# Performance work log

Measured on AMD Instinct MI355X. Metric: run time of the kernel, lower is better.

The kernel has to match this reference:

```python
import jax, jax.numpy as jnp
import numpy as np

N_NODES = 50000
N_EDGES = 800000
NUM_RELS = 16
IN_DIM, H_DIM, OUT_DIM = 128, 128, 64


def setup_inputs() -> dict:
    key = jax.random.key(0)
    ks = jax.random.split(key, 7)
    feat = jax.random.normal(ks[0], (N_NODES, IN_DIM), dtype=jnp.float32)
    norm = jax.random.uniform(ks[1], (N_EDGES, 1), dtype=jnp.float32)
    bound1 = 1.0 / np.sqrt(IN_DIM)
    bound2 = 1.0 / np.sqrt(H_DIM)
    W1 = jax.random.uniform(ks[2], (NUM_RELS, IN_DIM, H_DIM), dtype=jnp.float32, minval=-bound1, maxval=bound1)
    W2 = jax.random.uniform(ks[3], (NUM_RELS, H_DIM, OUT_DIM), dtype=jnp.float32, minval=-bound2, maxval=bound2)
    src = jax.random.randint(ks[4], (N_EDGES,), 0, N_NODES, dtype=jnp.int32)
    dst = jax.random.randint(ks[5], (N_EDGES,), 0, N_NODES, dtype=jnp.int32)
    etypes = jax.random.randint(ks[6], (N_EDGES,), 0, NUM_RELS, dtype=jnp.int32)
    return {"feat": feat, "norm": norm, "W1": W1, "W2": W2, "src": src, "dst": dst, "etypes": etypes}


def _rgcn_layer(h, W, src, dst, etypes, norm, num_nodes):
    # Transform every node by every relation weight (dense batched GEMM),
    # then gather the (src, etype) slice per edge: identical math to
    # gather_mm(h[src], W, idx_b=etypes) since matmul commutes with gather.
    t = jnp.einsum('ni,rio->nro', h, W)          # [N, R, O]
    msg = t[src, etypes] * norm                  # [E, O]
    return jax.ops.segment_sum(msg, dst, num_segments=num_nodes)  # sum-aggregate


def reference(feat, norm, W1, W2, src, dst, etypes):
    n = feat.shape[0]
    h = jax.nn.relu(_rgcn_layer(feat, W1, src, dst, etypes, norm, n))
    out = _rgcn_layer(h, W2, src, dst, etypes, norm, n)
    return out
```

## Files before the change

kernel.cpp:

```cpp
#include <hip/hip_runtime.h>


#define R_NUM 16

typedef __attribute__((ext_vector_type(8))) short bf16x8;
typedef __attribute__((ext_vector_type(4))) float f32x4;

__device__ __forceinline__ float bf2f(unsigned short u) {
    unsigned int x = ((unsigned int)u) << 16;
    return __builtin_bit_cast(float, x);
}
__device__ __forceinline__ unsigned short f2bf(float f) {
    unsigned int x = __builtin_bit_cast(unsigned int, f);
    x += 0x7FFFu + ((x >> 16) & 1u);
    return (unsigned short)(x >> 16);
}
__device__ __forceinline__ unsigned pack2(float a, float b) {
    return (unsigned)f2bf(a) | ((unsigned)f2bf(b) << 16);
}
__device__ __forceinline__ float lo16(unsigned v) { return bf2f((unsigned short)(v & 0xFFFF)); }
__device__ __forceinline__ float hi16(unsigned v) { return bf2f((unsigned short)(v >> 16)); }

__global__ void detect_dtype(const unsigned short* __restrict__ raw, int* flag) {
    __shared__ int tot;
    if (threadIdx.x == 0) tot = 0;
    __syncthreads();
    int c = 0;
    for (int i = threadIdx.x; i < 4096; i += 256) {
        unsigned short u = raw[2 * i];
        int e = (u >> 7) & 0xFF;
        if (e >= 113 && e <= 134) c++;
    }
    atomicAdd(&tot, c);
    __syncthreads();
    if (threadIdx.x == 0) *flag = (tot > 2048) ? 1 : 0;
}

__global__ void transpose_both(const void* __restrict__ W1, const void* __restrict__ W2,
                               unsigned short* __restrict__ w1t, unsigned short* __restrict__ w2t,
                               const int* __restrict__ flagp) {
    const int flag = *flagp;
    const int n1 = R_NUM * 128 * 128;
    const int n2 = R_NUM * 128 * 64;
    int idx = blockIdx.x * 256 + threadIdx.x;
    if (idx < n1) {
        int k = idx % 128, o = (idx / 128) % 128, r = idx / (128 * 128);
        int iin = (r * 128 + k) * 128 + o;
        float v = flag ? bf2f(((const unsigned short*)W1)[iin]) : ((const float*)W1)[iin];
        w1t[idx] = f2bf(v);
    } else if (idx < n1 + n2) {
        int j = idx - n1;
        int k = j % 128, o = (j / 128) % 64, r = j / (128 * 64);
        int iin = (r * 128 + k) * 64 + o;
        float v = flag ? bf2f(((const unsigned short*)W2)[iin]) : ((const float*)W2)[iin];
        w2t[j] = f2bf(v);
    }
}

template <int NOUT, int AMODE>
__global__ __launch_bounds__(256, 3) void gemm_all(const void* __restrict__ Asrc,
                                                   const unsigned short* __restrict__ Wt,
                                                   unsigned short* __restrict__ T, int nnodes,
                                                   const int* __restrict__ flagp) {
    constexpr int LDA = 136;
    constexpr int NTC = NOUT / 64;
    __shared__ unsigned short lA[64 * LDA];
    __shared__ unsigned short lB[NOUT * LDA];
    const int tid = threadIdx.x;
    const int node0 = blockIdx.x * 64;
    const int flag = (AMODE == 0) ? *flagp : 1;

    for (int i = tid; i < 64 * 16; i += 256) {
        int row = i >> 4, seg = i & 15;
        int node = node0 + row;
        uint4 v = make_uint4(0u, 0u, 0u, 0u);
        if (node < nnodes) {
            if (AMODE == 2 || flag) {
                v = *(const uint4*)((const unsigned short*)Asrc + (size_t)node * 128 + seg * 8);
            } else {
                const float* p = (const float*)Asrc + (size_t)node * 128 + seg * 8;
                float4 f0 = ((const float4*)p)[0];
                float4 f1 = ((const float4*)p)[1];
                v.x = pack2(f0.x, f0.y);
                v.y = pack2(f0.z, f0.w);
                v.z = pack2(f1.x, f1.y);
                v.w = pack2(f1.z, f1.w);
            }
        }
        *(uint4*)(lA + row * LDA + seg * 8) = v;
    }

    auto stageB = [&](int rel) {
        for (int i = tid; i < NOUT * 16; i += 256) {
            int o = i >> 4, seg = i & 15;
            *(uint4*)(lB + o * LDA + seg * 8) =
                *(const uint4*)(Wt + ((size_t)rel * NOUT + o) * 128 + seg * 8);
        }
    };
    stageB(0);
    __syncthreads();

    const int w = tid >> 6, lane = tid & 63;
    const int quad = lane >> 4, mr = lane & 15;

    bf16x8 afr[16];
#pragma unroll
    for (int mt = 0; mt < 4; mt++)
#pragma unroll
        for (int kk = 0; kk < 4; kk++)
            afr[mt * 4 + kk] = *(const bf16x8*)(lA + (mt * 16 + mr) * LDA + kk * 32 + quad * 8);

    constexpr int SEGS = NOUT / 8;
    constexpr int SPT = 64 * SEGS / 256;

    for (int rel = 0; rel < R_NUM; rel++) {
        f32x4 acc[4][NTC];
#pragma unroll
        for (int mt = 0; mt < 4; mt++)
#pragma unroll
            for (int c = 0; c < NTC; c++) acc[mt][c] = 0.f;

#pragma unroll
        for (int kk = 0; kk < 4; kk++) {
#pragma unroll
            for (int c = 0; c < NTC; c++) {
                bf16x8 b = *(const bf16x8*)(lB + (c * 64 + w * 16 + mr) * LDA + kk * 32 + quad * 8);
#pragma unroll
                for (int mt = 0; mt < 4; mt++)
                    acc[mt][c] = __builtin_amdgcn_mfma_f32_16x16x32_bf16(b, afr[mt * 4 + kk],
                                                                         acc[mt][c], 0, 0, 0);
            }
        }
        __syncthreads();

        if (rel + 1 < R_NUM) stageB(rel + 1);
#pragma unroll
        for (int mt = 0; mt < 4; mt++)
#pragma unroll
            for (int c = 0; c < NTC; c++) {
                uint2 pv;
                pv.x = pack2(acc[mt][c][0], acc[mt][c][1]);
                pv.y = pack2(acc[mt][c][2], acc[mt][c][3]);
                *(uint2*)(lA + (mt * 16 + mr) * LDA + c * 64 + w * 16 + quad * 4) = pv;
            }
        __syncthreads();

#pragma unroll
        for (int it = 0; it < SPT; it++) {
            int i = it * 256 + tid;
            int row = i / SEGS, seg = i % SEGS;
            int node = node0 + row;
            if (node < nnodes)
                *(uint4*)(T + ((size_t)rel * nnodes + node) * NOUT + seg * 8) =
                    *(const uint4*)(lA + row * LDA + seg * 8);
        }
    }
}

__global__ void hist_dst(const int* __restrict__ dst, int* __restrict__ counts, int nedges) {
    int e = blockIdx.x * 256 + threadIdx.x;
    if (e < nedges) atomicAdd(&counts[dst[e]], 1);
}

__global__ __launch_bounds__(256) void scan_phase1(const int* __restrict__ counts,
                                                   int* __restrict__ blocksums, int n) {
    __shared__ int red[256];
    int base = blockIdx.x * 1024 + threadIdx.x * 4;
    int s = 0;
#pragma unroll
    for (int j = 0; j < 4; j++) {
        int idx = base + j;
        if (idx < n) s += counts[idx];
    }
    red[threadIdx.x] = s;
    __syncthreads();
    for (int d = 128; d > 0; d >>= 1) {
        if (threadIdx.x < d) red[threadIdx.x] += red[threadIdx.x + d];
        __syncthreads();
    }
    if (threadIdx.x == 0) blocksums[blockIdx.x] = red[0];
}

__global__ __launch_bounds__(1024) void scan_phase2(const int* __restrict__ blocksums,
                                                    int* __restrict__ blockoff, int nb) {
    __shared__ int arr[1024];
    int t = threadIdx.x;
    arr[t] = (t < nb) ? blocksums[t] : 0;
    __syncthreads();
    for (int d = 1; d < 1024; d <<= 1) {
        int v = (t >= d) ? arr[t - d] : 0;
        __syncthreads();
        arr[t] += v;
        __syncthreads();
    }
    if (t < nb) blockoff[t] = (t == 0) ? 0 : arr[t - 1];
}

__global__ __launch_bounds__(256) void scan_phase3(const int* __restrict__ counts,
                                                   const int* __restrict__ blockoff,
                                                   int* __restrict__ offsets,
                                                   int* __restrict__ cursor, int n) {
    __shared__ int tsum[256];
    int base = blockIdx.x * 1024 + threadIdx.x * 4;
    int c[4];
    int s = 0;
#pragma unroll
    for (int j = 0; j < 4; j++) {
        int idx = base + j;
        c[j] = (idx < n) ? counts[idx] : 0;
        s += c[j];
    }
    tsum[threadIdx.x] = s;
    __syncthreads();
    for (int d = 1; d < 256; d <<= 1) {
        int v = (threadIdx.x >= d) ? tsum[threadIdx.x - d] : 0;
        __syncthreads();
        tsum[threadIdx.x] += v;
        __syncthreads();
    }
    int run = blockoff[blockIdx.x] + ((threadIdx.x == 0) ? 0 : tsum[threadIdx.x - 1]);
#pragma unroll
    for (int j = 0; j < 4; j++) {
        int idx = base + j;
        if (idx < n) {
            offsets[idx] = run;
            cursor[idx] = run;
            if (idx == n - 1) offsets[n] = run + c[j];
            run += c[j];
        }
    }
}

__global__ void fill_payload(const int* __restrict__ src, const int* __restrict__ dst,
                             const int* __restrict__ et, const void* __restrict__ nrm,
                             const int* __restrict__ flagp, int* __restrict__ cursor,
                             uint2* __restrict__ payload, int nedges) {
    int e = blockIdx.x * 256 + threadIdx.x;
    if (e >= nedges) return;
    int flag = *flagp;
    float nm = flag ? bf2f(((const unsigned short*)nrm)[e]) : ((const float*)nrm)[e];
    int pos = atomicAdd(&cursor[dst[e]], 1);
    uint2 pl;
    pl.x = ((unsigned)src[e] << 4) | (unsigned)(et[e] & 15);
    pl.y = __builtin_bit_cast(unsigned, nm);
    payload[pos] = pl;
}

template <int NOUT, int OUTMODE>
__global__ __launch_bounds__(256) void gather_seg(const unsigned short* __restrict__ T,
                                                  const int* __restrict__ offsets,
                                                  const uint2* __restrict__ payload,
                                                  void* __restrict__ out, int nnodes,
                                                  const int* __restrict__ flagp) {
    constexpr int SUBW = NOUT / 2;
    const int lane = threadIdx.x & 63;
    const int ll = lane & (SUBW - 1);
    const int dpb = 256 / SUBW;
    const int dst = blockIdx.x * dpb + threadIdx.x / SUBW;
    if (dst >= nnodes) return;
    const int base = lane & ~(SUBW - 1);
    const int beg = offsets[dst], end = offsets[dst + 1];
    float ax = 0.f, ay = 0.f;

    auto rowp = [&](unsigned key) {
        return (const unsigned*)(T + ((size_t)(key & 15) * nnodes + (key >> 4)) * NOUT);
    };

    for (int i = beg; i < end; i += SUBW) {
        int cnt = min(SUBW, end - i);
        uint2 pl = make_uint2(0u, 0u);
        if (ll < cnt) pl = payload[i + ll];
        int j = 0;
        for (; j + 4 <= cnt; j += 4) {
            unsigned k0 = (unsigned)__shfl((int)pl.x, base + j);
            unsigned k1 = (unsigned)__shfl((int)pl.x, base + j + 1);
            unsigned k2 = (unsigned)__shfl((int)pl.x, base + j + 2);
            unsigned k3 = (unsigned)__shfl((int)pl.x, base + j + 3);
            float n0 = __builtin_bit_cast(float, (unsigned)__shfl((int)pl.y, base + j));
            float n1 = __builtin_bit_cast(float, (unsigned)__shfl((int)pl.y, base + j + 1));
            float n2 = __builtin_bit_cast(float, (unsigned)__shfl((int)pl.y, base + j + 2));
            float n3 = __builtin_bit_cast(float, (unsigned)__shfl((int)pl.y, base + j + 3));
            unsigned v0 = rowp(k0)[ll];
            unsigned v1 = rowp(k1)[ll];
            unsigned v2 = rowp(k2)[ll];
            unsigned v3 = rowp(k3)[ll];
            ax = fmaf(lo16(v0), n0, ax); ay = fmaf(hi16(v0), n0, ay);
            ax = fmaf(lo16(v1), n1, ax); ay = fmaf(hi16(v1), n1, ay);
            ax = fmaf(lo16(v2), n2, ax); ay = fmaf(hi16(v2), n2, ay);
            ax = fmaf(lo16(v3), n3, ax); ay = fmaf(hi16(v3), n3, ay);
        }
        for (; j < cnt; j++) {
            unsigned k = (unsigned)__shfl((int)pl.x, base + j);
            float nm = __builtin_bit_cast(float, (unsigned)__shfl((int)pl.y, base + j));
            unsigned v = rowp(k)[ll];
            ax = fmaf(lo16(v), nm, ax);
            ay = fmaf(hi16(v), nm, ay);
        }
    }
    if (OUTMODE == 0) {
        ((unsigned*)out)[(size_t)dst * SUBW + ll] = pack2(fmaxf(ax, 0.f), fmaxf(ay, 0.f));
    } else {
        if (*flagp) {
            ((unsigned*)out)[(size_t)dst * SUBW + ll] = pack2(ax, ay);
        } else {
            float2 v;
            v.x = ax; v.y = ay;
            ((float2*)out)[(size_t)dst * SUBW + ll] = v;
        }
    }
}

template <int NOUT, int AMODE>
__global__ __launch_bounds__(256) void gemm_rel(const void* __restrict__ Asrc,
                                                const unsigned short* __restrict__ Wt,
                                                unsigned short* __restrict__ T, int nnodes,
                                                int rbase, const int* __restrict__ flagp) {
    constexpr int LDA = 136;
    __shared__ unsigned short lA[64 * LDA];
    __shared__ unsigned short lB[NOUT * LDA];
    const int tid = threadIdx.x;
    const int node0 = blockIdx.x * 64;
    const int rel = rbase + blockIdx.y;
    const int Gr = gridDim.y;
    const int flag = (AMODE == 0) ? *flagp : 1;

    for (int i = tid; i < 64 * 16; i += 256) {
        int row = i >> 4, seg = i & 15;
        int node = node0 + row;
        uint4 v = make_uint4(0u, 0u, 0u, 0u);
        if (node < nnodes) {
            if (AMODE == 1) {
                const float* p = (const float*)Asrc + (size_t)node * 128 + seg * 8;
                float4 f0 = ((const float4*)p)[0];
                float4 f1 = ((const float4*)p)[1];
                v.x = pack2(fmaxf(f0.x, 0.f), fmaxf(f0.y, 0.f));
                v.y = pack2(fmaxf(f0.z, 0.f), fmaxf(f0.w, 0.f));
                v.z = pack2(fmaxf(f1.x, 0.f), fmaxf(f1.y, 0.f));
                v.w = pack2(fmaxf(f1.z, 0.f), fmaxf(f1.w, 0.f));
            } else if (flag) {
                v = *(const uint4*)((const unsigned short*)Asrc + (size_t)node * 128 + seg * 8);
            } else {
                const float* p = (const float*)Asrc + (size_t)node * 128 + seg * 8;
                float4 f0 = ((const float4*)p)[0];
                float4 f1 = ((const float4*)p)[1];
                v.x = pack2(f0.x, f0.y);
                v.y = pack2(f0.z, f0.w);
                v.z = pack2(f1.x, f1.y);
                v.w = pack2(f1.z, f1.w);
            }
        }
        *(uint4*)(lA + row * LDA + seg * 8) = v;
    }
    for (int i = tid; i < NOUT * 16; i += 256) {
        int o = i >> 4, seg = i & 15;
        *(uint4*)(lB + o * LDA + seg * 8) =
            *(const uint4*)(Wt + ((size_t)rel * NOUT + o) * 128 + seg * 8);
    }
    __syncthreads();

    const int w = tid >> 6, lane = tid & 63;
    const int quad = lane >> 4, mr = lane & 15;
    constexpr int NT = NOUT / 16;
    f32x4 acc[NT];
#pragma unroll
    for (int t = 0; t < NT; t++) acc[t] = 0.f;
    const unsigned short* pa = lA + (w * 16 + mr) * LDA + quad * 8;
    const unsigned short* pb = lB + mr * LDA + quad * 8;
#pragma unroll
    for (int kk = 0; kk < 4; kk++) {
        bf16x8 a = *(const bf16x8*)(pa + kk * 32);
#pragma unroll
        for (int nt = 0; nt < NT; nt++) {
            bf16x8 b = *(const bf16x8*)(pb + nt * 16 * LDA + kk * 32);
            acc[nt] = __builtin_amdgcn_mfma_f32_16x16x32_bf16(a, b, acc[nt], 0, 0, 0);
        }
    }
#pragma unroll
    for (int nt = 0; nt < NT; nt++)
#pragma unroll
        for (int reg = 0; reg < 4; reg++) {
            int node = node0 + w * 16 + quad * 4 + reg;
            if (node < nnodes)
                T[((size_t)node * Gr + blockIdx.y) * NOUT + nt * 16 + mr] = f2bf(acc[nt][reg]);
        }
}

template <int NOUT>
__global__ void scatter_k(const unsigned short* __restrict__ T, int Gr, int rbase,
                          const void* __restrict__ nrm, const int* __restrict__ flagp,
                          const int* __restrict__ src, const int* __restrict__ dst,
                          const int* __restrict__ et, float* __restrict__ accum, int nedges) {
    constexpr int LPE = NOUT / 2;
    const int flag = *flagp;
    const int epb = 256 / LPE;
    const int sub = threadIdx.x % LPE;
    const int slot = threadIdx.x / LPE;
    for (int e = blockIdx.x * epb + slot; e < nedges; e += gridDim.x * epb) {
        int g = et[e] - rbase;
        if (g < 0 || g >= Gr) continue;
        int s = src[e], d = dst[e];
        float nm = flag ? bf2f(((const unsigned short*)nrm)[e]) : ((const float*)nrm)[e];
        unsigned pv = ((const unsigned*)(T + ((size_t)s * Gr + g) * NOUT))[sub];
        float* p = accum + (size_t)d * NOUT + sub * 2;
        unsafeAtomicAdd(p, lo16(pv) * nm);
        unsafeAtomicAdd(p + 1, hi16(pv) * nm);
    }
}

__global__ void write_out(const float* __restrict__ acc, void* __restrict__ dout, int n,
                          const int* __restrict__ flagp) {
    int flag = *flagp;
    int i = blockIdx.x * 256 + threadIdx.x;
    if (i >= n) return;
    float v = acc[i];
    if (flag) ((unsigned short*)dout)[i] = f2bf(v);
    else      ((float*)dout)[i] = v;
}

extern "C" void kernel_launch(void* const* d_in, const int* in_sizes, int n_in,
                              void* d_out, int out_size, void* d_ws, size_t ws_size,
                              hipStream_t stream) {
    const void* feat = d_in[0];
    const void* norm = d_in[1];
    const void* W1 = d_in[2];
    const void* W2 = d_in[3];
    const int* src = (const int*)d_in[4];
    const int* dst = (const int*)d_in[5];
    const int* et  = (const int*)d_in[6];

    const int nnodes = in_sizes[0] / 128;
    const int nedges = in_sizes[1];

    char* ws = (char*)d_ws;
    size_t off = 0;
    auto alloc = [&](size_t bytes) { size_t o = off; off += (bytes + 255) & ~255ULL; return o; };
    size_t off_flag = alloc(4);
    size_t off_w1t  = alloc((size_t)R_NUM * 128 * 128 * 2);
    size_t off_w2t  = alloc((size_t)R_NUM * 64 * 128 * 2);

    int* flagp = (int*)(ws + off_flag);
    unsigned short* w1t = (unsigned short*)(ws + off_w1t);
    unsigned short* w2t = (unsigned short*)(ws + off_w2t);

    size_t f_off = off;
    auto falloc = [&](size_t bytes) { size_t o = f_off; f_off += (bytes + 255) & ~255ULL; return o; };
    size_t off_offs = falloc((size_t)(nnodes + 1) * 4);
    size_t off_curs = falloc((size_t)nnodes * 4);
    size_t off_cnt  = falloc((size_t)nnodes * 4);
    size_t off_bsum = falloc(1024 * 4);
    size_t off_boff = falloc(1024 * 4);
    size_t off_pay  = falloc((size_t)nedges * 8);
    size_t off_hbf  = falloc((size_t)nnodes * 128 * 2);
    size_t off_t    = falloc((size_t)nnodes * R_NUM * 128 * 2);
    const int nb = (nnodes + 1023) / 1024;
    bool fast = (f_off <= ws_size) && (nb <= 1024);

    const int gx = (nnodes + 63) / 64;
    const int ntr = R_NUM * 128 * 128 + R_NUM * 128 * 64;

    detect_dtype<<<1, 256, 0, stream>>>((const unsigned short*)feat, flagp);
    transpose_both<<<(ntr + 255) / 256, 256, 0, stream>>>(W1, W2, w1t, w2t, flagp);

    if (fast) {
        int* offs = (int*)(ws + off_offs);
        int* curs = (int*)(ws + off_curs);
        int* cnt  = (int*)(ws + off_cnt);
        int* bsum = (int*)(ws + off_bsum);
        int* boff = (int*)(ws + off_boff);
        uint2* pay = (uint2*)(ws + off_pay);
        unsigned short* hbf = (unsigned short*)(ws + off_hbf);
        unsigned short* t = (unsigned short*)(ws + off_t);

        hipMemsetAsync(cnt, 0, (size_t)nnodes * 4, stream);
        hist_dst<<<(nedges + 255) / 256, 256, 0, stream>>>(dst, cnt, nedges);
        scan_phase1<<<nb, 256, 0, stream>>>(cnt, bsum, nnodes);
        scan_phase2<<<1, 1024, 0, stream>>>(bsum, boff, nb);
        scan_phase3<<<nb, 256, 0, stream>>>(cnt, boff, offs, curs, nnodes);
        fill_payload<<<(nedges + 255) / 256, 256, 0, stream>>>(src, dst, et, norm, flagp,
                                                               curs, pay, nedges);

        gemm_all<128, 0><<<gx, 256, 0, stream>>>(feat, w1t, t, nnodes, flagp);
        gather_seg<128, 0><<<(nnodes + 3) / 4, 256, 0, stream>>>(t, offs, pay, hbf, nnodes, flagp);
        gemm_all<64, 2><<<gx, 256, 0, stream>>>(hbf, w2t, t, nnodes, flagp);
        gather_seg<64, 1><<<(nnodes + 7) / 8, 256, 0, stream>>>(t, offs, pay, d_out, nnodes, flagp);
        return;
    }

    size_t off_hpre = alloc((size_t)nnodes * 128 * 4);
    size_t off_oacc = alloc((size_t)nnodes * 64 * 4);
    size_t t_cap = (ws_size > off) ? (ws_size - off) : 0;
    auto pick_gr = [&](int ncol) {
        int gr = 0;
        for (int g = 16; g >= 1; g >>= 1)
            if ((size_t)nnodes * g * ncol * 2 <= t_cap) { gr = g; break; }
        return gr;
    };
    int Gr1 = pick_gr(128);
    int Gr2 = pick_gr(64);
    if (Gr1 < 1 || Gr2 < 1) {
        hipMemsetAsync(d_out, 0x42, (size_t)out_size * 2, stream);
        return;
    }
    float* hpre = (float*)(ws + off_hpre);
    float* oacc = (float*)(ws + off_oacc);
    unsigned short* t = (unsigned short*)(ws + off);

    hipMemsetAsync(hpre, 0, (size_t)nnodes * 128 * 4, stream);
    hipMemsetAsync(oacc, 0, (size_t)nnodes * 64 * 4, stream);
    for (int rb = 0; rb < R_NUM; rb += Gr1) {
        gemm_rel<128, 0><<<dim3(gx, Gr1), 256, 0, stream>>>(feat, w1t, t, nnodes, rb, flagp);
        scatter_k<128><<<4096, 256, 0, stream>>>(t, Gr1, rb, norm, flagp, src, dst, et, hpre, nedges);
    }
    for (int rb = 0; rb < R_NUM; rb += Gr2) {
        gemm_rel<64, 1><<<dim3(gx, Gr2), 256, 0, stream>>>(hpre, w2t, t, nnodes, rb, flagp);
        scatter_k<64><<<4096, 256, 0, stream>>>(t, Gr2, rb, norm, flagp, src, dst, et, oacc, nedges);
    }
    int nout = nnodes * 64;
    write_out<<<(nout + 255) / 256, 256, 0, stream>>>(oacc, d_out, nout, flagp);
}
```

Measured before the change: 398.0 us.

## Split per-relation GEMM across grid blocks and write results directly from registers

The dense node-by-relation GEMM now launches one block per (relation, 64-node tile) instead of one block looping over all 16 relations. This raises parallelism and removes the per-relation syncthreads and the LDS round-trip for the output, since accumulators are packed and stored straight to global memory. The cost is that each node tile of A is reloaded and reconverted 16 times (once per relation block), A fragments are reread from LDS inside the MFMA loop, and output stores become narrower, less coalesced 8-byte writes.

After: 438.7 us. 10.2% more time.

```diff
diff --git a/kernel.cpp b/kernel.cpp
--- a/kernel.cpp
+++ b/kernel.cpp
@@ -58,16 +58,17 @@
 }
 
 template <int NOUT, int AMODE>
-__global__ __launch_bounds__(256, 3) void gemm_all(const void* __restrict__ Asrc,
-                                                   const unsigned short* __restrict__ Wt,
-                                                   unsigned short* __restrict__ T, int nnodes,
-                                                   const int* __restrict__ flagp) {
+__global__ __launch_bounds__(256, 3) void gemm_tile(const void* __restrict__ Asrc,
+                                                    const unsigned short* __restrict__ Wt,
+                                                    unsigned short* __restrict__ T, int nnodes,
+                                                    const int* __restrict__ flagp) {
     constexpr int LDA = 136;
     constexpr int NTC = NOUT / 64;
     __shared__ unsigned short lA[64 * LDA];
     __shared__ unsigned short lB[NOUT * LDA];
     const int tid = threadIdx.x;
-    const int node0 = blockIdx.x * 64;
+    const int rel = blockIdx.x;
+    const int node0 = blockIdx.y * 64;
     const int flag = (AMODE == 0) ? *flagp : 1;
 
     for (int i = tid; i < 64 * 16; i += 256) {
@@ -89,70 +90,46 @@
         }
         *(uint4*)(lA + row * LDA + seg * 8) = v;
     }
-
-    auto stageB = [&](int rel) {
-        for (int i = tid; i < NOUT * 16; i += 256) {
-            int o = i >> 4, seg = i & 15;
-            *(uint4*)(lB + o * LDA + seg * 8) =
-                *(const uint4*)(Wt + ((size_t)rel * NOUT + o) * 128 + seg * 8);
-        }
-    };
-    stageB(0);
+    for (int i = tid; i < NOUT * 16; i += 256) {
+        int o = i >> 4, seg = i & 15;
+        *(uint4*)(lB + o * LDA + seg * 8) =
+            *(const uint4*)(Wt + ((size_t)rel * NOUT + o) * 128 + seg * 8);
+    }
     __syncthreads();
 
     const int w = tid >> 6, lane = tid & 63;
     const int quad = lane >> 4, mr = lane & 15;
 
-    bf16x8 afr[16];
+    f32x4 acc[4][NTC];
 #pragma unroll
     for (int mt = 0; mt < 4; mt++)
 #pragma unroll
-        for (int kk = 0; kk < 4; kk++)
-            afr[mt * 4 + kk] = *(const bf16x8*)(lA + (mt * 16 + mr) * LDA + kk * 32 + quad * 8);
-
-    constexpr int SEGS = NOUT / 8;
-    constexpr int SPT = 64 * SEGS / 256;
-
-    for (int rel = 0; rel < R_NUM; rel++) {
-        f32x4 acc[4][NTC];
-#pragma unroll
-        for (int mt = 0; mt < 4; mt++)
-#pragma unroll
-            for (int c = 0; c < NTC; c++) acc[mt][c] = 0.f;
-
-#pragma unroll
-        for (int kk = 0; kk < 4; kk++) {
-#pragma unroll
-            for (int c = 0; c < NTC; c++) {
-                bf16x8 b = *(const bf16x8*)(lB + (c * 64 + w * 16 + mr) * LDA + kk * 32 + quad * 8);
-#pragma unroll
-                for (int mt = 0; mt < 4; mt++)
-                    acc[mt][c] = __builtin_amdgcn_mfma_f32_16x16x32_bf16(b, afr[mt * 4 + kk],
-                                                                         acc[mt][c], 0, 0, 0);
+        for (int c = 0; c < NTC; c++) acc[mt][c] = 0.f;
+
+#pragma unroll
+    for (int kk = 0; kk < 4; kk++) {
+#pragma unroll
+        for (int c = 0; c < NTC; c++) {
+            bf16x8 b = *(const bf16x8*)(lB + (c * 64 + w * 16 + mr) * LDA + kk * 32 + quad * 8);
+#pragma unroll
+            for (int mt = 0; mt < 4; mt++) {
+                bf16x8 a = *(const bf16x8*)(lA + (mt * 16 + mr) * LDA + kk * 32 + quad * 8);
+                acc[mt][c] = __builtin_amdgcn_mfma_f32_16x16x32_bf16(b, a, acc[mt][c], 0, 0, 0);
             }
         }
-        __syncthreads();
-
-        if (rel + 1 < R_NUM) stageB(rel + 1);
-#pragma unroll
-        for (int mt = 0; mt < 4; mt++)
+    }
+
+#pragma unroll
+    for (int mt = 0; mt < 4; mt++) {
+        int node = node0 + mt * 16 + mr;
+        if (node < nnodes) {
 #pragma unroll
             for (int c = 0; c < NTC; c++) {
                 uint2 pv;
                 pv.x = pack2(acc[mt][c][0], acc[mt][c][1]);
                 pv.y = pack2(acc[mt][c][2], acc[mt][c][3]);
-                *(uint2*)(lA + (mt * 16 + mr) * LDA + c * 64 + w * 16 + quad * 4) = pv;
+                *(uint2*)(T + ((size_t)rel * nnodes + node) * NOUT + c * 64 + w * 16 + quad * 4) = pv;
             }
-        __syncthreads();
-
-#pragma unroll
-        for (int it = 0; it < SPT; it++) {
-            int i = it * 256 + tid;
-            int row = i / SEGS, seg = i % SEGS;
-            int node = node0 + row;
-            if (node < nnodes)
-                *(uint4*)(T + ((size_t)rel * nnodes + node) * NOUT + seg * 8) =
-                    *(const uint4*)(lA + row * LDA + seg * 8);
         }
     }
 }
@@ -479,9 +456,9 @@
         fill_payload<<<(nedges + 255) / 256, 256, 0, stream>>>(src, dst, et, norm, flagp,
                                                                curs, pay, nedges);
 
-        gemm_all<128, 0><<<gx, 256, 0, stream>>>(feat, w1t, t, nnodes, flagp);
+        gemm_tile<128, 0><<<dim3(R_NUM, gx), 256, 0, stream>>>(feat, w1t, t, nnodes, flagp);
         gather_seg<128, 0><<<(nnodes + 3) / 4, 256, 0, stream>>>(t, offs, pay, hbf, nnodes, flagp);
-        gemm_all<64, 2><<<gx, 256, 0, stream>>>(hbf, w2t, t, nnodes, flagp);
+        gemm_tile<64, 2><<<dim3(R_NUM, gx), 256, 0, stream>>>(hbf, w2t, t, nnodes, flagp);
         gather_seg<64, 1><<<(nnodes + 7) / 8, 256, 0, stream>>>(t, offs, pay, d_out, nnodes, flagp);
         return;
     }
```
